# Kernel optimization log

Hardware: AMD Instinct MI355X
Metric: run time of the kernel (lower is better)

## Reference

```python
import jax, jax.numpy as jnp
import numpy as np

N = 8192
IN_DIM = 512
OUT_DIM = 512
TASK_DIM = 64
NEG_INF = -9.0e15  # matches torch's -9000000000000000.0 mask value


def setup_inputs() -> dict:
    key = jax.random.key(0)
    ks = jax.random.split(key, 12)
    def lin(k, fan_in, fan_out):
        kw, kb = jax.random.split(k)
        bound = 1.0 / np.sqrt(fan_in)
        W = jax.random.uniform(kw, (fan_in, fan_out), minval=-bound, maxval=bound, dtype=jnp.float32)
        b = jax.random.uniform(kb, (fan_out,), minval=-bound, maxval=bound, dtype=jnp.float32)
        return W, b
    h = jax.random.normal(ks[0], (N, IN_DIM), dtype=jnp.float32)
    z = jax.random.normal(ks[1], (N, TASK_DIM), dtype=jnp.float32)
    adj = jax.random.randint(ks[2], (N, N), 0, 2, dtype=jnp.int32)
    Wm, bm = lin(ks[3], IN_DIM, OUT_DIM)
    Wg, bg = lin(ks[4], IN_DIM + TASK_DIM, OUT_DIM)
    Wk, bk = lin(ks[5], IN_DIM, OUT_DIM)
    Wq, bq = lin(ks[6], OUT_DIM, OUT_DIM)
    a = jax.random.normal(ks[7], (OUT_DIM * 2, 1), dtype=jnp.float32)
    return {"h": h, "adj": adj, "z": z, "Wm": Wm, "bm": bm, "Wg": Wg, "bg": bg,
            "Wk": Wk, "bk": bk, "Wq": Wq, "bq": bq, "a": a}


def reference(h, adj, z, Wm, bm, Wg, bg, Wk, bk, Wq, bq, a):
    # raw message + task-conditioned gate
    raw_message = jax.nn.relu(h @ Wm + bm)                       # [N, D]
    gate = jax.nn.sigmoid(jnp.concatenate([h, z], axis=1) @ Wg + bg)  # [N, D]
    gated_message = gate * raw_message                           # [N, D]
    gate_l1_loss = jnp.sum(jnp.abs(gate)) / gate.size
    # attention scores: e[i,j] = leaky_relu(k_j . a[:D] + q_i . a[D:])
    # (decomposes the [N,N,2D] concat @ a without materializing it)
    q = gated_message @ Wq + bq                                  # [N, D]
    k = h @ Wk + bk                                              # [N, D]
    sk = k @ a[:OUT_DIM, 0]                                      # [N] key term (varies over j)
    sq = q @ a[OUT_DIM:, 0]                                      # [N] query term (varies over i)
    e = jax.nn.leaky_relu(sq[:, None] + sk[None, :])             # [N, N]
    attention = jnp.where(adj > 0, e, NEG_INF)
    attention = jax.nn.softmax(attention, axis=1)                # [N, N]
    agg_message = attention.T @ gated_message                    # [N, D]
    h_new = (agg_message + h) / 2
    return h_new, gate_l1_loss
```

## Files before the change

### kernel.cpp

```cpp
#include <hip/hip_runtime.h>

typedef unsigned short u16;
typedef unsigned char u8;
typedef unsigned long long u64;
typedef short s16x8 __attribute__((ext_vector_type(8)));
typedef float f32x4 __attribute__((ext_vector_type(4)));
typedef int i32x4 __attribute__((ext_vector_type(4)));
typedef int i32x8 __attribute__((ext_vector_type(8)));

#define NN 8192
#define DD 512
#define KCAT 576

__device__ __forceinline__ u16 f2bf(float f) {
  unsigned u = __float_as_uint(f);
  unsigned r = u + 0x7fffu + ((u >> 16) & 1u);
  return (u16)(r >> 16);
}
__device__ __forceinline__ float bf2f(u16 s) {
  return __uint_as_float(((unsigned)s) << 16);
}
__device__ __forceinline__ void gld16(const void* g, void* l) {
  __builtin_amdgcn_global_load_lds((const __attribute__((address_space(1))) void*)g,
                                   (__attribute__((address_space(3))) void*)l, 16, 0, 0);
}
__device__ __forceinline__ int pk8(float f0, float f1, float f2, float f3) {
  int p = __builtin_amdgcn_cvt_pk_fp8_f32(f0, f1, 0, 0);
  p = __builtin_amdgcn_cvt_pk_fp8_f32(f2, f3, p, 1);
  return p;
}

__global__ void k_prep(const float* __restrict__ Wk, const float* __restrict__ Wq,
                       const float* __restrict__ bk, const float* __restrict__ bq,
                       const float* __restrict__ a, const float* __restrict__ Wm,
                       const float* __restrict__ Wg, const float* __restrict__ h,
                       const float* __restrict__ z, float* __restrict__ wk_a,
                       float* __restrict__ wq_a, float* __restrict__ sc,
                       u16* __restrict__ WcT, u16* __restrict__ X) {
  const int b = blockIdx.x, t = threadIdx.x;
  if (b < 5) {
    if (b < 2) {
      int c = b * 256 + t;
      float s = 0.f;
      for (int d = 0; d < 512; d++) s += Wk[(size_t)c * 512 + d] * a[d];
      wk_a[c] = s;
    } else if (b < 4) {
      int c = (b - 2) * 256 + t;
      float s = 0.f;
      for (int d = 0; d < 512; d++) s += Wq[(size_t)c * 512 + d] * a[512 + d];
      wq_a[c] = s;
    } else {
      __shared__ float red[8];
      int lane = t & 63, w = t >> 6;
      float s1 = bk[t] * a[t] + bk[t + 256] * a[t + 256];
      float s2 = bq[t] * a[512 + t] + bq[t + 256] * a[768 + t];
      #pragma unroll
      for (int o = 32; o >= 1; o >>= 1) { s1 += __shfl_down(s1, o); s2 += __shfl_down(s2, o); }
      if (lane == 0) { red[w] = s1; red[4 + w] = s2; }
      __syncthreads();
      if (t == 0) {
        sc[0] = red[0] + red[1] + red[2] + red[3];
        sc[1] = red[4] + red[5] + red[6] + red[7];
      }
    }
  } else if (b < 293) {
    int tid = (b - 5) * 256 + t;
    int n = tid / 72, g = tid % 72;
    int lg = (g & ~7) | ((g & 7) ^ (n & 7));
    int k0 = lg * 8;
    s16x8 o;
    #pragma unroll
    for (int e = 0; e < 8; e++) {
      int k = k0 + e;
      float val;
      if (n < 512) val = (k < 512) ? Wm[(size_t)k * 512 + n] : 0.f;
      else         val = Wg[(size_t)k * 512 + (n - 512)];
      o[e] = (short)f2bf(val);
    }
    *(s16x8*)&WcT[(size_t)n * KCAT + g * 8] = o;
  } else {
    int tid = (b - 293) * 256 + t;
    int i = tid / 72, g = tid % 72;
    int lg = (g & ~7) | ((g & 7) ^ (i & 7));
    int k0 = lg * 8;
    s16x8 o;
    if (k0 < 512) {
      const f32x4* s = (const f32x4*)(h + (size_t)i * 512 + k0);
      f32x4 v0 = s[0], v1 = s[1];
      #pragma unroll
      for (int e = 0; e < 4; e++) { o[e] = (short)f2bf(v0[e]); o[e + 4] = (short)f2bf(v1[e]); }
    } else {
      const f32x4* s = (const f32x4*)(z + (size_t)i * 64 + (k0 - 512));
      f32x4 v0 = s[0], v1 = s[1];
      #pragma unroll
      for (int e = 0; e < 4; e++) { o[e] = (short)f2bf(v0[e]); o[e + 4] = (short)f2bf(v1[e]); }
    }
    *(s16x8*)&X[(size_t)i * KCAT + g * 8] = o;
  }
}

__global__ __launch_bounds__(256) void k_gp(const u16* __restrict__ X,
    const u16* __restrict__ W, const float* __restrict__ bm, const float* __restrict__ bg,
    u16* __restrict__ rm, u16* __restrict__ gate, float* __restrict__ l1part,
    const int* __restrict__ adj, u64* __restrict__ bits) {
  __shared__ __align__(16) u16 As[128 * 64];
  __shared__ __align__(16) u16 Bs[128 * 64];
  __shared__ float red[4];
  const int t = threadIdx.x, bid = blockIdx.x;
  if (bid < 512) {
    const int i0 = (bid & 63) * 128, n0 = (bid >> 6) * 128;
    const int lane = t & 63, w = t >> 6;
    const int lr = lane & 15, lh = lane >> 4;
    const int wm = (w >> 1) * 64, wn = (w & 1) * 64;
    const f32x4 vz = {0.f, 0.f, 0.f, 0.f};
    f32x4 acc[4][4];
    #pragma unroll
    for (int a_ = 0; a_ < 4; a_++)
      #pragma unroll
      for (int b_ = 0; b_ < 4; b_++) acc[a_][b_] = vz;

    for (int step = 0; step < 9; step++) {
      const int kk = step * 64;
      __syncthreads();
      #pragma unroll
      for (int c = 0; c < 4; c++) {
        int L = c * 256 + t;
        int row = L >> 3, ch = L & 7;
        gld16(X + (size_t)(i0 + row) * KCAT + kk + ch * 8, &As[L * 8]);
        gld16(W + (size_t)(n0 + row) * KCAT + kk + ch * 8, &Bs[L * 8]);
      }
      asm volatile("s_waitcnt vmcnt(0)" ::: "memory");
      __syncthreads();
      #pragma unroll
      for (int ks = 0; ks < 2; ks++) {
        s16x8 af[4], bfv[4];
        #pragma unroll
        for (int mr = 0; mr < 4; mr++) {
          int row = wm + mr * 16 + lr;
          int ch = (ks * 4 + lh) ^ (row & 7);
          af[mr] = *(const s16x8*)&As[row * 64 + ch * 8];
        }
        #pragma unroll
        for (int nr = 0; nr < 4; nr++) {
          int nn = wn + nr * 16 + lr;
          int ch = (ks * 4 + lh) ^ (nn & 7);
          bfv[nr] = *(const s16x8*)&Bs[nn * 64 + ch * 8];
        }
        #pragma unroll
        for (int mr = 0; mr < 4; mr++)
          #pragma unroll
          for (int nr = 0; nr < 4; nr++)
            acc[mr][nr] = __builtin_amdgcn_mfma_f32_16x16x32_bf16(af[mr], bfv[nr], acc[mr][nr], 0, 0, 0);
      }
    }
    float lsum = 0.f;
    #pragma unroll
    for (int nr = 0; nr < 4; nr++) {
      int nn = n0 + wn + nr * 16 + lr;
      bool ismsg = nn < 512;
      float bias = ismsg ? bm[nn] : bg[nn - 512];
      #pragma unroll
      for (int mr = 0; mr < 4; mr++) {
        #pragma unroll
        for (int r = 0; r < 4; r++) {
          int row = i0 + wm + mr * 16 + lh * 4 + r;
          float v0 = acc[mr][nr][r] + bias;
          if (ismsg) {
            rm[(size_t)row * 512 + nn] = f2bf(fmaxf(v0, 0.f));
          } else {
            float g = 1.f / (1.f + __expf(-v0));
            gate[(size_t)row * 512 + (nn - 512)] = f2bf(g);
            lsum += g;
          }
        }
      }
    }
    const int lane2 = t & 63, w2 = t >> 6;
    #pragma unroll
    for (int o = 32; o >= 1; o >>= 1) lsum += __shfl_down(lsum, o);
    if (lane2 == 0) red[w2] = lsum;
    __syncthreads();
    if (t == 0) l1part[bid] = red[0] + red[1] + red[2] + red[3];
  } else {
    u16* nib = As;
    const size_t i = bid - 512;
    #pragma unroll
    for (int k = 0; k < 2; k++) {
      const int4* src = (const int4*)(adj + i * NN + (size_t)(t + 256 * k) * 16);
      unsigned m = 0;
      #pragma unroll
      for (int q = 0; q < 4; q++) {
        int4 v = src[q];
        m |= (v.x > 0 ? 1u : 0u) << (4 * q);
        m |= (v.y > 0 ? 2u : 0u) << (4 * q);
        m |= (v.z > 0 ? 4u : 0u) << (4 * q);
        m |= (v.w > 0 ? 8u : 0u) << (4 * q);
      }
      nib[k * 256 + t] = (u16)m;
    }
    __syncthreads();
    if (t < 128) bits[i * 128 + t] = *(const u64*)&nib[t * 4];
  }
}

__global__ __launch_bounds__(256) void k_gemm1(const u16* __restrict__ X,
    const u16* __restrict__ W, const float* __restrict__ bm, const float* __restrict__ bg,
    u16* __restrict__ rm, u16* __restrict__ gate, float* __restrict__ l1part) {
  __shared__ __align__(16) u16 As[128 * 64];
  __shared__ __align__(16) u16 Bs[128 * 64];
  __shared__ float red[4];
  const int t = threadIdx.x, bid = blockIdx.x;
  const int i0 = (bid & 63) * 128, n0 = (bid >> 6) * 128;
  const int lane = t & 63, w = t >> 6;
  const int lr = lane & 15, lh = lane >> 4;
  const int wm = (w >> 1) * 64, wn = (w & 1) * 64;
  const f32x4 vz = {0.f, 0.f, 0.f, 0.f};
  f32x4 acc[4][4];
  #pragma unroll
  for (int a_ = 0; a_ < 4; a_++)
    #pragma unroll
    for (int b_ = 0; b_ < 4; b_++) acc[a_][b_] = vz;

  for (int step = 0; step < 9; step++) {
    const int kk = step * 64;
    __syncthreads();
    #pragma unroll
    for (int c = 0; c < 4; c++) {
      int L = c * 256 + t;
      int row = L >> 3, ch = L & 7;
      gld16(X + (size_t)(i0 + row) * KCAT + kk + ch * 8, &As[L * 8]);
      gld16(W + (size_t)(n0 + row) * KCAT + kk + ch * 8, &Bs[L * 8]);
    }
    asm volatile("s_waitcnt vmcnt(0)" ::: "memory");
    __syncthreads();
    #pragma unroll
    for (int ks = 0; ks < 2; ks++) {
      s16x8 af[4], bfv[4];
      #pragma unroll
      for (int mr = 0; mr < 4; mr++) {
        int row = wm + mr * 16 + lr;
        int ch = (ks * 4 + lh) ^ (row & 7);
        af[mr] = *(const s16x8*)&As[row * 64 + ch * 8];
      }
      #pragma unroll
      for (int nr = 0; nr < 4; nr++) {
        int nn = wn + nr * 16 + lr;
        int ch = (ks * 4 + lh) ^ (nn & 7);
        bfv[nr] = *(const s16x8*)&Bs[nn * 64 + ch * 8];
      }
      #pragma unroll
      for (int mr = 0; mr < 4; mr++)
        #pragma unroll
        for (int nr = 0; nr < 4; nr++)
          acc[mr][nr] = __builtin_amdgcn_mfma_f32_16x16x32_bf16(af[mr], bfv[nr], acc[mr][nr], 0, 0, 0);
    }
  }
  float lsum = 0.f;
  #pragma unroll
  for (int nr = 0; nr < 4; nr++) {
    int nn = n0 + wn + nr * 16 + lr;
    bool ismsg = nn < 512;
    float bias = ismsg ? bm[nn] : bg[nn - 512];
    #pragma unroll
    for (int mr = 0; mr < 4; mr++) {
      #pragma unroll
      for (int r = 0; r < 4; r++) {
        int row = i0 + wm + mr * 16 + lh * 4 + r;
        float v0 = acc[mr][nr][r] + bias;
        if (ismsg) {
          rm[(size_t)row * 512 + nn] = f2bf(fmaxf(v0, 0.f));
        } else {
          float g = 1.f / (1.f + __expf(-v0));
          gate[(size_t)row * 512 + (nn - 512)] = f2bf(g);
          lsum += g;
        }
      }
    }
  }
  #pragma unroll
  for (int o = 32; o >= 1; o >>= 1) lsum += __shfl_down(lsum, o);
  if (lane == 0) red[w] = lsum;
  __syncthreads();
  if (t == 0) l1part[bid] = red[0] + red[1] + red[2] + red[3];
}

__global__ __launch_bounds__(256) void k_rowact(const u16* __restrict__ rm,
    const u16* __restrict__ gate, const float* __restrict__ h,
    const float* __restrict__ wk_a, const float* __restrict__ wq_a,
    const float* __restrict__ sc, u16* __restrict__ gm, float* __restrict__ skv,
    float* __restrict__ sqv, float* __restrict__ uu, float* __restrict__ vv) {
  __shared__ float red[8];
  const int i = blockIdx.x, t = threadIdx.x;
  const int lane = t & 63, w = t >> 6;
  float sqp = 0.f, skp = 0.f;
  #pragma unroll
  for (int rep = 0; rep < 2; rep++) {
    int d = rep * 256 + t;
    float g = bf2f(gate[(size_t)i * 512 + d]);
    float r = bf2f(rm[(size_t)i * 512 + d]);
    float p = g * r;
    gm[(size_t)i * 512 + d] = f2bf(p);
    sqp += p * wq_a[d];
    skp += h[(size_t)i * 512 + d] * wk_a[d];
  }
  #pragma unroll
  for (int o = 32; o >= 1; o >>= 1) { sqp += __shfl_down(sqp, o); skp += __shfl_down(skp, o); }
  if (lane == 0) { red[w] = skp; red[4 + w] = sqp; }
  __syncthreads();
  if (t == 0) {
    float skt = red[0] + red[1] + red[2] + red[3] + sc[0];
    float sqt = red[4] + red[5] + red[6] + red[7] + sc[1];
    skv[i] = skt; sqv[i] = sqt;
    uu[i] = __expf(skt); vv[i] = __expf(0.01f * skt);
  }
}

__global__ __launch_bounds__(256) void k_tbs(const u64* __restrict__ bits,
    const float* __restrict__ sk, const float* __restrict__ uu, const float* __restrict__ vv,
    const float* __restrict__ sq, float* __restrict__ P, float* __restrict__ Q,
    const u16* __restrict__ gm, u8* __restrict__ gmT8, u64* __restrict__ bitT) {
  __shared__ __align__(16) u16 tile[64][72];
  const int bid = blockIdx.x, t = threadIdx.x;
  if (bid < 2048) {
    const int lane = t & 63, wv = t >> 6;
    const int i = bid * 4 + wv;
    const float sqi = sq[i];
    const float nsq = -sqi;
    const u64* brow = bits + (size_t)i * 128;
    float zp = 0.f, zn = 0.f, m_loc = -3.0e38f;
    for (int k = 0; k < 128; k++) {
      u64 word = brow[k];
      float skj = sk[k * 64 + lane];
      float uj = uu[k * 64 + lane];
      float vj = vv[k * 64 + lane];
      m_loc = fmaxf(m_loc, skj);
      bool msk = (word >> lane) & 1ULL;
      bool pos = skj > nsq;
      zp += (msk && pos) ? uj : 0.f;
      zn += (msk && !pos) ? vj : 0.f;
    }
    #pragma unroll
    for (int o = 32; o >= 1; o >>= 1) {
      zp += __shfl_down(zp, o);
      zn += __shfl_down(zn, o);
      m_loc = fmaxf(m_loc, __shfl_down(m_loc, o));
    }
    if (lane == 0) {
      float xk = sqi + m_loc;
      float m_i = xk >= 0.f ? xk : 0.01f * xk;
      float ep = __expf(sqi - m_i), en = __expf(0.01f * sqi - m_i);
      float Z = ep * zp + en * zn;
      float inv = 1.0f / Z;
      P[i] = ep * inv;
      Q[i] = en * inv;
    }
  } else if (bid < 3072) {
    const int b2 = bid - 2048;
    const int ti = b2 & 127, td = b2 >> 7;
    #pragma unroll
    for (int rep = 0; rep < 2; rep++) {
      int L = rep * 256 + t;
      int row = L >> 3, ch = L & 7;
      s16x8 val = *(const s16x8*)(gm + (size_t)(ti * 64 + row) * 512 + td * 64 + ch * 8);
      *(s16x8*)&tile[row][ch * 8] = val;
    }
    __syncthreads();
    const int dl = t >> 2, lc = t & 3;
    const int d = td * 64 + dl;
    const int chg = ti * 4 + lc;
    i32x4 o;
    #pragma unroll
    for (int q = 0; q < 4; q++) {
      int ib = lc * 16 + q * 4;
      o[q] = pk8(bf2f(tile[ib][dl]) * 16.f, bf2f(tile[ib + 1][dl]) * 16.f,
                 bf2f(tile[ib + 2][dl]) * 16.f, bf2f(tile[ib + 3][dl]) * 16.f);
    }
    *(i32x4*)(gmT8 + (size_t)d * NN + (chg >> 3) * 128 + ((chg & 7) ^ (d & 7)) * 16) = o;
  } else {
    int wid = (bid - 3072) * 4 + (t >> 6);
    int ti = wid & 127, tj = wid >> 7;
    int lane = t & 63;
    u64 w = bits[(size_t)(ti * 64 + lane) * 128 + tj];
    u64 out = 0;
    #pragma unroll
    for (int jj = 0; jj < 64; jj++) {
      u64 b = __ballot((int)((w >> jj) & 1ULL));
      if (jj == lane) out = b;
    }
    bitT[(size_t)(tj * 64 + lane) * 128 + ti] = out;
  }
}

__global__ void k_bitT(const u64* __restrict__ bits, u64* __restrict__ bitT) {
  int wid = blockIdx.x * 4 + (threadIdx.x >> 6);
  int ti = wid & 127, tj = wid >> 7;
  int lane = threadIdx.x & 63;
  u64 w = bits[(size_t)(ti * 64 + lane) * 128 + tj];
  u64 out = 0;
  #pragma unroll
  for (int jj = 0; jj < 64; jj++) {
    u64 b = __ballot((int)((w >> jj) & 1ULL));
    if (jj == lane) out = b;
  }
  bitT[(size_t)(tj * 64 + lane) * 128 + ti] = out;
}

__global__ __launch_bounds__(256) void k_tgm(const u16* __restrict__ gm, u16* __restrict__ gmT) {
  __shared__ __align__(16) u16 tile[64][72];
  const int bid = blockIdx.x;
  const int ti = bid & 127, td = bid >> 7;
  const int t = threadIdx.x;
  #pragma unroll
  for (int rep = 0; rep < 2; rep++) {
    int L = rep * 256 + t;
    int row = L >> 3, ch = L & 7;
    s16x8 val = *(const s16x8*)(gm + (size_t)(ti * 64 + row) * 512 + td * 64 + ch * 8);
    *(s16x8*)&tile[row][ch * 8] = val;
  }
  __syncthreads();
  #pragma unroll
  for (int rep = 0; rep < 2; rep++) {
    int L = rep * 256 + t;
    int dr = L >> 3, ig = L & 7;
    int d = td * 64 + dr;
    s16x8 o;
    #pragma unroll
    for (int e = 0; e < 8; e++) o[e] = (short)tile[ig * 8 + e][dr];
    *(s16x8*)(gmT + (size_t)d * NN + ti * 64 + (ig ^ (d & 7)) * 8) = o;
  }
}

__global__ __launch_bounds__(256) void k_rowstats(const int* __restrict__ adj,
    const float* __restrict__ sk, const float* __restrict__ sq,
    u64* __restrict__ bits, float* __restrict__ P, float* __restrict__ Q) {
  __shared__ float sks[NN];
  __shared__ u64 bw[128];
  __shared__ float red[8];
  const int i = blockIdx.x, t = threadIdx.x;
  const int lane = t & 63, w = t >> 6;
  const int* arow = adj + (size_t)i * NN;
  float kmax = -3.0e38f;
  for (int c = 0; c < 32; c++) {
    int j = c * 256 + t;
    int av = arow[j];
    float skj = sk[j];
    sks[j] = skj;
    bool bit = av > 0;
    u64 m = __ballot(bit);
    if (lane == 0) bw[c * 4 + w] = m;
    if (bit) kmax = fmaxf(kmax, skj);
  }
  #pragma unroll
  for (int o = 32; o >= 1; o >>= 1) kmax = fmaxf(kmax, __shfl_down(kmax, o));
  if (lane == 0) red[w] = kmax;
  __syncthreads();
  float K = fmaxf(fmaxf(red[0], red[1]), fmaxf(red[2], red[3]));
  float sqi = sq[i];
  float xk = sqi + K;
  float m_i = xk >= 0.f ? xk : 0.01f * xk;
  float s = 0.f;
  for (int c = 0; c < 32; c++) {
    int j = c * 256 + t;
    u64 mw = bw[c * 4 + w];
    float xx = sqi + sks[j];
    float f = xx >= 0.f ? xx : 0.01f * xx;
    float e = __expf(f - m_i);
    if ((mw >> lane) & 1ULL) s += e;
  }
  #pragma unroll
  for (int o = 32; o >= 1; o >>= 1) s += __shfl_down(s, o);
  if (lane == 0) red[4 + w] = s;
  __syncthreads();
  if (t == 0) {
    float Z = red[4] + red[5] + red[6] + red[7];
    float inv = 1.0f / Z;
    P[i] = __expf(sqi - m_i) * inv;
    Q[i] = __expf(0.01f * sqi - m_i) * inv;
  }
  if (t < 128) bits[(size_t)i * 128 + t] = bw[t];
}

__global__ __launch_bounds__(256) void k_attgen8(const u64* __restrict__ bitT,
    const float* __restrict__ P, const float* __restrict__ Q, const float* __restrict__ sq,
    const float* __restrict__ u, const float* __restrict__ v, const float* __restrict__ sk,
    u8* __restrict__ attT8) {
  const int t = threadIdx.x, bid = blockIdx.x;
  const int jt = bid >> 1, ih = bid & 1;
  const int j0 = jt * 16;
  const int i0 = ih * 4096 + t * 16;
  f32x4 Pv[4], Qv[4], Sv[4];
  #pragma unroll
  for (int q = 0; q < 4; q++) {
    Pv[q] = *(const f32x4*)(P + i0 + q * 4);
    Qv[q] = *(const f32x4*)(Q + i0 + q * 4);
    Sv[q] = *(const f32x4*)(sq + i0 + q * 4);
  }
  const int widx = i0 >> 6;
  const int bsh = (t & 3) * 16;
  const int chg = i0 >> 4;
  const int wnd = chg >> 3, cs = chg & 7;
  #pragma unroll 2
  for (int r = 0; r < 16; r++) {
    const int j = j0 + r;
    const float uj = u[j] * 256.f, vj = v[j] * 256.f, nskj = -sk[j];
    const u64 w64 = bitT[(size_t)j * 128 + widx];
    const unsigned m16 = (unsigned)(w64 >> bsh) & 0xFFFFu;
    i32x4 o;
    #pragma unroll
    for (int q = 0; q < 4; q++) {
      float f[4];
      #pragma unroll
      for (int e = 0; e < 4; e++) {
        bool pos = Sv[q][e] > nskj;
        float val = pos ? Pv[q][e] * uj : Qv[q][e] * vj;
        f[e] = ((m16 >> (q * 4 + e)) & 1u) ? val : 0.f;
      }
      o[q] = pk8(f[0], f[1], f[2], f[3]);
    }
    *(i32x4*)(attT8 + (size_t)j * NN + wnd * 128 + ((cs ^ (j & 7)) * 16)) = o;
  }
}

__device__ __forceinline__ i32x8 ld_frag8(const u8* base, int row, int lh) {
  const int c0 = ((2 * lh) ^ (row & 7)) * 16;
  const int c1 = ((2 * lh + 1) ^ (row & 7)) * 16;
  i32x4 lo = *(const i32x4*)(base + row * 128 + c0);
  i32x4 hi = *(const i32x4*)(base + row * 128 + c1);
  i32x8 r;
  r[0] = lo[0]; r[1] = lo[1]; r[2] = lo[2]; r[3] = lo[3];
  r[4] = hi[0]; r[5] = hi[1]; r[6] = hi[2]; r[7] = hi[3];
  return r;
}

__global__ __launch_bounds__(256) void k_aggr8(const u8* __restrict__ attT8,
    const u8* __restrict__ gmT8, u16* __restrict__ pb) {
  __shared__ __align__(16) u8 As[128 * 128];
  __shared__ __align__(16) u8 Bs[128 * 128];
  const int t = threadIdx.x, bid = blockIdx.x;
  const int lid = (bid & 7) * 128 + (bid >> 3);
  const int dt = lid & 3, jt = (lid >> 2) & 63, split = lid >> 8;
  const int j0 = jt * 128, d0 = dt * 128;
  const int lane = t & 63, w = t >> 6;
  const int lr = lane & 15, lh = lane >> 4;
  const int wm = (w >> 1) * 64, wn = (w & 1) * 64;
  const f32x4 vz = {0.f, 0.f, 0.f, 0.f};
  f32x4 acc[4][4];
  #pragma unroll
  for (int a_ = 0; a_ < 4; a_++)
    #pragma unroll
    for (int b_ = 0; b_ < 4; b_++) acc[a_][b_] = vz;

  for (int step = 0; step < 16; step++) {
    const int ss = split * 16 + step;
    __syncthreads();
    #pragma unroll
    for (int c = 0; c < 4; c++) {
      int idx = c * 256 + t;
      int row = idx >> 3, ch = idx & 7;
      gld16(attT8 + (size_t)(j0 + row) * NN + (size_t)ss * 128 + ch * 16, &As[idx * 16]);
      gld16(gmT8 + (size_t)(d0 + row) * NN + (size_t)ss * 128 + ch * 16, &Bs[idx * 16]);
    }
    asm volatile("s_waitcnt vmcnt(0)" ::: "memory");
    __syncthreads();
    i32x8 af[4], bfv[4];
    #pragma unroll
    for (int mr = 0; mr < 4; mr++) af[mr] = ld_frag8(As, wm + mr * 16 + lr, lh);
    #pragma unroll
    for (int nr = 0; nr < 4; nr++) bfv[nr] = ld_frag8(Bs, wn + nr * 16 + lr, lh);
    #pragma unroll
    for (int mr = 0; mr < 4; mr++)
      #pragma unroll
      for (int nr = 0; nr < 4; nr++)
        acc[mr][nr] = __builtin_amdgcn_mfma_scale_f32_16x16x128_f8f6f4(
            af[mr], bfv[nr], acc[mr][nr], 0, 0,
            0, 0x77777777,
            0, 0x7B7B7B7B);
  }
  u16* pbs = pb + (size_t)split * NN * 512;
  #pragma unroll
  for (int mr = 0; mr < 4; mr++) {
    #pragma unroll
    for (int nr = 0; nr < 4; nr++) {
      int dn = d0 + wn + nr * 16 + lr;
      #pragma unroll
      for (int r = 0; r < 4; r++) {
        int jj = j0 + wm + mr * 16 + lh * 4 + r;
        pbs[(size_t)jj * 512 + dn] = f2bf(acc[mr][nr][r]);
      }
    }
  }
}

__global__ __launch_bounds__(512) void k_aggr(const u16* __restrict__ gmT,
    const u64* __restrict__ bitT, const float* __restrict__ P, const float* __restrict__ Q,
    const float* __restrict__ sq, const float* __restrict__ u, const float* __restrict__ v,
    const float* __restrict__ sk, u16* __restrict__ pb) {
  __shared__ __align__(16) u16 Alds[128 * 64];
  __shared__ __align__(16) u16 Blds[128 * 64];
  const int t = threadIdx.x, bid = blockIdx.x;
  const int lid = (bid & 7) * 128 + (bid >> 3);
  const int j_t = lid & 63, rest = lid >> 6;
  const int split = rest & 3, d_t = rest >> 2;
  const int j0 = j_t * 128, d0 = d_t * 128;
  const int lane = t & 63, w = t >> 6;
  const int lr = lane & 15, lh = lane >> 4;
  const int wm = (w >> 1) * 32, wn = (w & 1) * 64;
  const int gj = t & 127, gq = t >> 7;
  const int jg = j0 + gj;
  const float uj = u[jg], vj = v[jg], nskj = -sk[jg];
  const u64* btrow = bitT + (size_t)jg * 128;
  const f32x4 vzero = {0.f, 0.f, 0.f, 0.f};
  f32x4 acc[2][4];
  #pragma unroll
  for (int a_ = 0; a_ < 2; a_++)
    #pragma unroll
    for (int b_ = 0; b_ < 4; b_++) acc[a_][b_] = vzero;

  for (int step = 0; step < 32; step++) {
    const int ss = split * 32 + step;
    __syncthreads();
    #pragma unroll
    for (int c = 0; c < 2; c++) {
      int L = c * 512 + t;
      int dd = L >> 3, ch = L & 7;
      gld16(gmT + (size_t)(d0 + dd) * NN + ss * 64 + ch * 8, &Blds[L * 8]);
    }
    u64 word = btrow[ss];
    #pragma unroll
    for (int cc = 0; cc < 2; cc++) {
      int ig = gq + cc * 4;
      int i8 = ss * 64 + ig * 8;
      const f32x4* P4 = (const f32x4*)(P + i8);
      const f32x4* Q4 = (const f32x4*)(Q + i8);
      const f32x4* S4 = (const f32x4*)(sq + i8);
      s16x8 rr;
      #pragma unroll
      for (int hf = 0; hf < 2; hf++) {
        f32x4 pv = P4[hf], qv = Q4[hf], sv = S4[hf];
        #pragma unroll
        for (int e = 0; e < 4; e++) {
          int ie = hf * 4 + e;
          float val = (sv[e] > nskj) ? pv[e] * uj : qv[e] * vj;
          bool bit = (word >> (ig * 8 + ie)) & 1ULL;
          rr[ie] = bit ? (short)f2bf(val) : (short)0;
        }
      }
      *(s16x8*)&Alds[gj * 64 + (ig ^ (gj & 7)) * 8] = rr;
    }
    asm volatile("s_waitcnt vmcnt(0)" ::: "memory");
    __syncthreads();
    #pragma unroll
    for (int ks = 0; ks < 2; ks++) {
      s16x8 af[2], bfv[4];
      #pragma unroll
      for (int mr = 0; mr < 2; mr++) {
        int row = wm + mr * 16 + lr;
        int ch = (ks * 4 + lh) ^ (row & 7);
        af[mr] = *(const s16x8*)&Alds[row * 64 + ch * 8];
      }
      #pragma unroll
      for (int nr = 0; nr < 4; nr++) {
        int dn = wn + nr * 16 + lr;
        int ch = (ks * 4 + lh) ^ (dn & 7);
        bfv[nr] = *(const s16x8*)&Blds[dn * 64 + ch * 8];
      }
      #pragma unroll
      for (int mr = 0; mr < 2; mr++)
        #pragma unroll
        for (int nr = 0; nr < 4; nr++)
          acc[mr][nr] = __builtin_amdgcn_mfma_f32_16x16x32_bf16(af[mr], bfv[nr], acc[mr][nr], 0, 0, 0);
    }
  }
  u16* pbs = pb + (size_t)split * NN * 512;
  #pragma unroll
  for (int mr = 0; mr < 2; mr++) {
    #pragma unroll
    for (int nr = 0; nr < 4; nr++) {
      int dn = d0 + wn + nr * 16 + lr;
      #pragma unroll
      for (int r = 0; r < 4; r++) {
        int jj = j0 + wm + mr * 16 + lh * 4 + r;
        pbs[(size_t)jj * 512 + dn] = f2bf(acc[mr][nr][r]);
      }
    }
  }
}

__global__ __launch_bounds__(256) void k_reduce(const u16* __restrict__ pb,
    const float* __restrict__ h, const float* __restrict__ part, float* __restrict__ out) {
  if (blockIdx.x == 2048) {
    __shared__ float red[4];
    int t = threadIdx.x, lane = t & 63, w = t >> 6;
    float s = part[t] + part[t + 256];
    #pragma unroll
    for (int o = 32; o >= 1; o >>= 1) s += __shfl_down(s, o);
    if (lane == 0) red[w] = s;
    __syncthreads();
    if (t == 0) out[(size_t)NN * 512] = (red[0] + red[1] + red[2] + red[3]) * (1.0f / 4194304.0f);
    return;
  }
  size_t base = ((size_t)blockIdx.x * 256 + threadIdx.x) * 8;
  s16x8 p0 = *(const s16x8*)(pb + base);
  s16x8 p1 = *(const s16x8*)(pb + (size_t)NN * 512 + base);
  s16x8 p2 = *(const s16x8*)(pb + (size_t)2 * NN * 512 + base);
  s16x8 p3 = *(const s16x8*)(pb + (size_t)3 * NN * 512 + base);
  f32x4 h0 = *(const f32x4*)(h + base);
  f32x4 h1 = *(const f32x4*)(h + base + 4);
  f32x4 o0, o1;
  #pragma unroll
  for (int e = 0; e < 4; e++) {
    o0[e] = (bf2f((u16)p0[e]) + bf2f((u16)p1[e]) + bf2f((u16)p2[e]) + bf2f((u16)p3[e]) + h0[e]) * 0.5f;
    o1[e] = (bf2f((u16)p0[e + 4]) + bf2f((u16)p1[e + 4]) + bf2f((u16)p2[e + 4]) + bf2f((u16)p3[e + 4]) + h1[e]) * 0.5f;
  }
  *(f32x4*)(out + base) = o0;
  *(f32x4*)(out + base + 4) = o1;
}

extern "C" void kernel_launch(void* const* d_in, const int* in_sizes, int n_in,
                              void* d_out, int out_size, void* d_ws, size_t ws_size,
                              hipStream_t stream) {
  const float* h  = (const float*)d_in[0];
  const int*   adj= (const int*)d_in[1];
  const float* z  = (const float*)d_in[2];
  const float* Wm = (const float*)d_in[3];
  const float* bm = (const float*)d_in[4];
  const float* Wg = (const float*)d_in[5];
  const float* bg = (const float*)d_in[6];
  const float* Wk = (const float*)d_in[7];
  const float* bk = (const float*)d_in[8];
  const float* Wq = (const float*)d_in[9];
  const float* bq = (const float*)d_in[10];
  const float* a  = (const float*)d_in[11];
  float* out = (float*)d_out;
  char* ws = (char*)d_ws;

  size_t off = 0;
  auto alloc = [&](size_t b) { size_t o = off; off += (b + 255) & ~(size_t)255; return o; };
  float* wk_a = (float*)(ws + alloc(512 * 4));
  float* wq_a = (float*)(ws + alloc(512 * 4));
  float* sc   = (float*)(ws + alloc(256));
  float* skv  = (float*)(ws + alloc(NN * 4));
  float* sqv  = (float*)(ws + alloc(NN * 4));
  float* uu   = (float*)(ws + alloc(NN * 4));
  float* vv   = (float*)(ws + alloc(NN * 4));
  float* Pp   = (float*)(ws + alloc(NN * 4));
  float* Qp   = (float*)(ws + alloc(NN * 4));
  float* l1p  = (float*)(ws + alloc(512 * 4));
  u16*   WcT  = (u16*)(ws + alloc((size_t)1024 * KCAT * 2));
  u16*   gmTb = (u16*)(ws + alloc((size_t)DD * NN * 2));
  u64*   bitTb= (u64*)(ws + alloc((size_t)NN * 128 * 8));
  u64*   bitsB= (u64*)(ws + alloc((size_t)NN * 128 * 8));
  u16*   pb   = (u16*)(ws + alloc((size_t)4 * NN * 512 * 2));

  const size_t bigNeed = (size_t)NN * NN * 2;
  bool bigPath = (ws_size >= off + bigNeed);

  if (bigPath) {
    char* big = ws + alloc(bigNeed);
    u16* Xbf  = (u16*)big;
    u16* rm   = (u16*)(big + ((size_t)10 << 20));
    u16* gate = (u16*)(big + ((size_t)19 << 20));
    u16* gm   = (u16*)(big + ((size_t)28 << 20));
    u8*  attT8= (u8*)big;
    u8*  gmT8 = (u8*)gmTb;

    k_prep<<<2597, 256, 0, stream>>>(Wk, Wq, bk, bq, a, Wm, Wg, h, z,
                                     wk_a, wq_a, sc, WcT, Xbf);
    k_gp<<<8704, 256, 0, stream>>>(Xbf, WcT, bm, bg, rm, gate, l1p, adj, bitsB);
    k_rowact<<<8192, 256, 0, stream>>>(rm, gate, h, wk_a, wq_a, sc, gm, skv, sqv, uu, vv);
    k_tbs<<<7168, 256, 0, stream>>>(bitsB, skv, uu, vv, sqv, Pp, Qp, gm, gmT8, bitTb);
    k_attgen8<<<1024, 256, 0, stream>>>(bitTb, Pp, Qp, sqv, uu, vv, skv, attT8);
    k_aggr8<<<1024, 256, 0, stream>>>(attT8, gmT8, pb);
    k_reduce<<<2049, 256, 0, stream>>>(pb, h, l1p, out);
  } else {
    char* regA = ws + alloc((size_t)NN * KCAT * 2);
    char* regB = ws + alloc((size_t)NN * 512 * 2);
    char* regC = ws + alloc((size_t)NN * 512 * 2);
    u16* Xbf = (u16*)regA;  u64* bits = (u64*)regA;
    u16* rm  = (u16*)regB;
    u16* gate= (u16*)regC;
    u16* gmv = (u16*)(ws + alloc((size_t)NN * 512 * 2));
    k_prep<<<2597, 256, 0, stream>>>(Wk, Wq, bk, bq, a, Wm, Wg, h, z,
                                     wk_a, wq_a, sc, WcT, Xbf);
    k_gemm1<<<512, 256, 0, stream>>>(Xbf, WcT, bm, bg, rm, gate, l1p);
    k_rowact<<<8192, 256, 0, stream>>>(rm, gate, h, wk_a, wq_a, sc, gmv, skv, sqv, uu, vv);
    k_tgm<<<1024, 256, 0, stream>>>(gmv, gmTb);
    k_rowstats<<<8192, 256, 0, stream>>>(adj, skv, sqv, bits, Pp, Qp);
    k_bitT<<<4096, 256, 0, stream>>>(bits, bitTb);
    k_aggr<<<1024, 512, 0, stream>>>(gmTb, bitTb, Pp, Qp, sqv, uu, vv, skv, pb);
    k_reduce<<<2049, 256, 0, stream>>>(pb, h, l1p, out);
  }
}
```

Before: 231.0 us.

## Regroup mid-pipeline kernels: fuse bit transpose into rowact, gm transpose into attgen

Moves the adjacency bit-matrix transpose into the row-activation kernel and the gm-to-fp8 transpose into the attention-generation kernel, leaving the row softmax statistics as a standalone kernel. Attention generation now runs 8 rows per block instead of 16, so it uses 2048 blocks. The gm buffer is moved to a 80MB offset so the fused attgen kernel can write attT8 without overwriting gm while the transpose still reads it. The aim is to balance work across launches and fill otherwise idle waves. The cost is heterogeneous blocks within one launch.

```diff
diff --git a/kernel.cpp b/kernel.cpp
--- a/kernel.cpp
+++ b/kernel.cpp
@@ -284,6 +284,53 @@
   if (t == 0) l1part[bid] = red[0] + red[1] + red[2] + red[3];
 }
 
+__global__ __launch_bounds__(256) void k_rowbit(const u16* __restrict__ rm,
+    const u16* __restrict__ gate, const float* __restrict__ h,
+    const float* __restrict__ wk_a, const float* __restrict__ wq_a,
+    const float* __restrict__ sc, u16* __restrict__ gm, float* __restrict__ skv,
+    float* __restrict__ sqv, float* __restrict__ uu, float* __restrict__ vv,
+    const u64* __restrict__ bits, u64* __restrict__ bitT) {
+  __shared__ float red[8];
+  const int bid = blockIdx.x, t = threadIdx.x;
+  if (bid < 8192) {
+    const int i = bid;
+    const int lane = t & 63, w = t >> 6;
+    float sqp = 0.f, skp = 0.f;
+    #pragma unroll
+    for (int rep = 0; rep < 2; rep++) {
+      int d = rep * 256 + t;
+      float g = bf2f(gate[(size_t)i * 512 + d]);
+      float r = bf2f(rm[(size_t)i * 512 + d]);
+      float p = g * r;
+      gm[(size_t)i * 512 + d] = f2bf(p);
+      sqp += p * wq_a[d];
+      skp += h[(size_t)i * 512 + d] * wk_a[d];
+    }
+    #pragma unroll
+    for (int o = 32; o >= 1; o >>= 1) { sqp += __shfl_down(sqp, o); skp += __shfl_down(skp, o); }
+    if (lane == 0) { red[w] = skp; red[4 + w] = sqp; }
+    __syncthreads();
+    if (t == 0) {
+      float skt = red[0] + red[1] + red[2] + red[3] + sc[0];
+      float sqt = red[4] + red[5] + red[6] + red[7] + sc[1];
+      skv[i] = skt; sqv[i] = sqt;
+      uu[i] = __expf(skt); vv[i] = __expf(0.01f * skt);
+    }
+  } else {
+    int wid = (bid - 8192) * 4 + (t >> 6);
+    int ti = wid & 127, tj = wid >> 7;
+    int lane = t & 63;
+    u64 w = bits[(size_t)(ti * 64 + lane) * 128 + tj];
+    u64 out = 0;
+    #pragma unroll
+    for (int jj = 0; jj < 64; jj++) {
+      u64 b = __ballot((int)((w >> jj) & 1ULL));
+      if (jj == lane) out = b;
+    }
+    bitT[(size_t)(tj * 64 + lane) * 128 + ti] = out;
+  }
+}
+
 __global__ __launch_bounds__(256) void k_rowact(const u16* __restrict__ rm,
     const u16* __restrict__ gate, const float* __restrict__ h,
     const float* __restrict__ wk_a, const float* __restrict__ wq_a,
@@ -315,46 +362,85 @@
   }
 }
 
-__global__ __launch_bounds__(256) void k_tbs(const u64* __restrict__ bits,
+__global__ __launch_bounds__(256) void k_stats(const u64* __restrict__ bits,
     const float* __restrict__ sk, const float* __restrict__ uu, const float* __restrict__ vv,
-    const float* __restrict__ sq, float* __restrict__ P, float* __restrict__ Q,
-    const u16* __restrict__ gm, u8* __restrict__ gmT8, u64* __restrict__ bitT) {
+    const float* __restrict__ sq, float* __restrict__ P, float* __restrict__ Q) {
+  const int t = threadIdx.x, lane = t & 63, wv = t >> 6;
+  const int i = blockIdx.x * 4 + wv;
+  const float sqi = sq[i];
+  const float nsq = -sqi;
+  const u64* brow = bits + (size_t)i * 128;
+  float zp = 0.f, zn = 0.f, m_loc = -3.0e38f;
+  for (int k = 0; k < 128; k++) {
+    u64 word = brow[k];
+    float skj = sk[k * 64 + lane];
+    float uj = uu[k * 64 + lane];
+    float vj = vv[k * 64 + lane];
+    m_loc = fmaxf(m_loc, skj);
+    bool msk = (word >> lane) & 1ULL;
+    bool pos = skj > nsq;
+    zp += (msk && pos) ? uj : 0.f;
+    zn += (msk && !pos) ? vj : 0.f;
+  }
+  #pragma unroll
+  for (int o = 32; o >= 1; o >>= 1) {
+    zp += __shfl_down(zp, o);
+    zn += __shfl_down(zn, o);
+    m_loc = fmaxf(m_loc, __shfl_down(m_loc, o));
+  }
+  if (lane == 0) {
+    float xk = sqi + m_loc;
+    float m_i = xk >= 0.f ? xk : 0.01f * xk;
+    float ep = __expf(sqi - m_i), en = __expf(0.01f * sqi - m_i);
+    float Z = ep * zp + en * zn;
+    float inv = 1.0f / Z;
+    P[i] = ep * inv;
+    Q[i] = en * inv;
+  }
+}
+
+__global__ __launch_bounds__(256) void k_atg(const u64* __restrict__ bitT,
+    const float* __restrict__ P, const float* __restrict__ Q, const float* __restrict__ sq,
+    const float* __restrict__ u, const float* __restrict__ v, const float* __restrict__ sk,
+    u8* __restrict__ attT8, const u16* __restrict__ gm, u8* __restrict__ gmT8) {
   __shared__ __align__(16) u16 tile[64][72];
-  const int bid = blockIdx.x, t = threadIdx.x;
+  const int t = threadIdx.x, bid = blockIdx.x;
   if (bid < 2048) {
-    const int lane = t & 63, wv = t >> 6;
-    const int i = bid * 4 + wv;
-    const float sqi = sq[i];
-    const float nsq = -sqi;
-    const u64* brow = bits + (size_t)i * 128;
-    float zp = 0.f, zn = 0.f, m_loc = -3.0e38f;
-    for (int k = 0; k < 128; k++) {
-      u64 word = brow[k];
-      float skj = sk[k * 64 + lane];
-      float uj = uu[k * 64 + lane];
-      float vj = vv[k * 64 + lane];
-      m_loc = fmaxf(m_loc, skj);
-      bool msk = (word >> lane) & 1ULL;
-      bool pos = skj > nsq;
-      zp += (msk && pos) ? uj : 0.f;
-      zn += (msk && !pos) ? vj : 0.f;
-    }
-    #pragma unroll
-    for (int o = 32; o >= 1; o >>= 1) {
-      zp += __shfl_down(zp, o);
-      zn += __shfl_down(zn, o);
-      m_loc = fmaxf(m_loc, __shfl_down(m_loc, o));
-    }
-    if (lane == 0) {
-      float xk = sqi + m_loc;
-      float m_i = xk >= 0.f ? xk : 0.01f * xk;
-      float ep = __expf(sqi - m_i), en = __expf(0.01f * sqi - m_i);
-      float Z = ep * zp + en * zn;
-      float inv = 1.0f / Z;
-      P[i] = ep * inv;
-      Q[i] = en * inv;
-    }
-  } else if (bid < 3072) {
+    const int jt = bid >> 1, ih = bid & 1;
+    const int j0 = jt * 8;
+    const int i0 = ih * 4096 + t * 16;
+    f32x4 Pv[4], Qv[4], Sv[4];
+    #pragma unroll
+    for (int q = 0; q < 4; q++) {
+      Pv[q] = *(const f32x4*)(P + i0 + q * 4);
+      Qv[q] = *(const f32x4*)(Q + i0 + q * 4);
+      Sv[q] = *(const f32x4*)(sq + i0 + q * 4);
+    }
+    const int widx = i0 >> 6;
+    const int bsh = (t & 3) * 16;
+    const int chg = i0 >> 4;
+    const int wnd = chg >> 3, cs = chg & 7;
+    #pragma unroll 2
+    for (int r = 0; r < 8; r++) {
+      const int j = j0 + r;
+      const float uj = u[j] * 256.f, vj = v[j] * 256.f, nskj = -sk[j];
+      const u64 w64 = bitT[(size_t)j * 128 + widx];
+      const unsigned m16 = (unsigned)(w64 >> bsh) & 0xFFFFu;
+      i32x4 o;
+      #pragma unroll
+      for (int q = 0; q < 4; q++) {
+        float f[4];
+        #pragma unroll
+        for (int e = 0; e < 4; e++) {
+          bool pos = Sv[q][e] > nskj;
+          float val = pos ? Pv[q][e] * uj : Qv[q][e] * vj;
+          f[e] = ((m16 >> (q * 4 + e)) & 1u) ? val : 0.f;
+        }
+        o[q] = pk8(f[0], f[1], f[2], f[3]);
+      }
+      *(i32x4*)(attT8 + (size_t)j * NN + wnd * 128 + ((cs ^ (j & 7)) * 16)) = o;
+    }
+  } else {
     const int b2 = bid - 2048;
     const int ti = b2 & 127, td = b2 >> 7;
     #pragma unroll
@@ -376,18 +462,6 @@
                  bf2f(tile[ib + 2][dl]) * 16.f, bf2f(tile[ib + 3][dl]) * 16.f);
     }
     *(i32x4*)(gmT8 + (size_t)d * NN + (chg >> 3) * 128 + ((chg & 7) ^ (d & 7)) * 16) = o;
-  } else {
-    int wid = (bid - 3072) * 4 + (t >> 6);
-    int ti = wid & 127, tj = wid >> 7;
-    int lane = t & 63;
-    u64 w = bits[(size_t)(ti * 64 + lane) * 128 + tj];
-    u64 out = 0;
-    #pragma unroll
-    for (int jj = 0; jj < 64; jj++) {
-      u64 b = __ballot((int)((w >> jj) & 1ULL));
-      if (jj == lane) out = b;
-    }
-    bitT[(size_t)(tj * 64 + lane) * 128 + ti] = out;
   }
 }
 
@@ -478,47 +552,6 @@
     Q[i] = __expf(0.01f * sqi - m_i) * inv;
   }
   if (t < 128) bits[(size_t)i * 128 + t] = bw[t];
-}
-
-__global__ __launch_bounds__(256) void k_attgen8(const u64* __restrict__ bitT,
-    const float* __restrict__ P, const float* __restrict__ Q, const float* __restrict__ sq,
-    const float* __restrict__ u, const float* __restrict__ v, const float* __restrict__ sk,
-    u8* __restrict__ attT8) {
-  const int t = threadIdx.x, bid = blockIdx.x;
-  const int jt = bid >> 1, ih = bid & 1;
-  const int j0 = jt * 16;
-  const int i0 = ih * 4096 + t * 16;
-  f32x4 Pv[4], Qv[4], Sv[4];
-  #pragma unroll
-  for (int q = 0; q < 4; q++) {
-    Pv[q] = *(const f32x4*)(P + i0 + q * 4);
-    Qv[q] = *(const f32x4*)(Q + i0 + q * 4);
-    Sv[q] = *(const f32x4*)(sq + i0 + q * 4);
-  }
-  const int widx = i0 >> 6;
-  const int bsh = (t & 3) * 16;
-  const int chg = i0 >> 4;
-  const int wnd = chg >> 3, cs = chg & 7;
-  #pragma unroll 2
-  for (int r = 0; r < 16; r++) {
-    const int j = j0 + r;
-    const float uj = u[j] * 256.f, vj = v[j] * 256.f, nskj = -sk[j];
-    const u64 w64 = bitT[(size_t)j * 128 + widx];
-    const unsigned m16 = (unsigned)(w64 >> bsh) & 0xFFFFu;
-    i32x4 o;
-    #pragma unroll
-    for (int q = 0; q < 4; q++) {
-      float f[4];
-      #pragma unroll
-      for (int e = 0; e < 4; e++) {
-        bool pos = Sv[q][e] > nskj;
-        float val = pos ? Pv[q][e] * uj : Qv[q][e] * vj;
-        f[e] = ((m16 >> (q * 4 + e)) & 1u) ? val : 0.f;
-      }
-      o[q] = pk8(f[0], f[1], f[2], f[3]);
-    }
-    *(i32x4*)(attT8 + (size_t)j * NN + wnd * 128 + ((cs ^ (j & 7)) * 16)) = o;
-  }
 }
 
 __device__ __forceinline__ i32x8 ld_frag8(const u8* base, int row, int lh) {
@@ -760,16 +793,17 @@
     u16* Xbf  = (u16*)big;
     u16* rm   = (u16*)(big + ((size_t)10 << 20));
     u16* gate = (u16*)(big + ((size_t)19 << 20));
-    u16* gm   = (u16*)(big + ((size_t)28 << 20));
+    u16* gm   = (u16*)(big + ((size_t)80 << 20));
     u8*  attT8= (u8*)big;
     u8*  gmT8 = (u8*)gmTb;
 
     k_prep<<<2597, 256, 0, stream>>>(Wk, Wq, bk, bq, a, Wm, Wg, h, z,
                                      wk_a, wq_a, sc, WcT, Xbf);
     k_gp<<<8704, 256, 0, stream>>>(Xbf, WcT, bm, bg, rm, gate, l1p, adj, bitsB);
-    k_rowact<<<8192, 256, 0, stream>>>(rm, gate, h, wk_a, wq_a, sc, gm, skv, sqv, uu, vv);
-    k_tbs<<<7168, 256, 0, stream>>>(bitsB, skv, uu, vv, sqv, Pp, Qp, gm, gmT8, bitTb);
-    k_attgen8<<<1024, 256, 0, stream>>>(bitTb, Pp, Qp, sqv, uu, vv, skv, attT8);
+    k_rowbit<<<12288, 256, 0, stream>>>(rm, gate, h, wk_a, wq_a, sc, gm, skv, sqv, uu, vv,
+                                        bitsB, bitTb);
+    k_stats<<<2048, 256, 0, stream>>>(bitsB, skv, uu, vv, sqv, Pp, Qp);
+    k_atg<<<3072, 256, 0, stream>>>(bitTb, Pp, Qp, sqv, uu, vv, skv, attT8, gm, gmT8);
     k_aggr8<<<1024, 256, 0, stream>>>(attT8, gmT8, pb);
     k_reduce<<<2049, 256, 0, stream>>>(pb, h, l1p, out);
   } else {
```

After: 231.9 us. No clear change (+0.4%).
